# Performance work log

Hardware: AMD Instinct MI355X
Metric: run time of the kernel (lower is better)

Reference implementation:

```python
import jax, jax.numpy as jnp
import numpy as np

NUM_HEADS = 8


def setup_inputs() -> dict:
    key = jax.random.key(0)
    ks = jax.random.split(key, 5)
    b, c, h, w = 8, 256, 32, 32
    x = jax.random.normal(ks[0], (b, c, h, w), dtype=jnp.float32)
    w_qkv = jax.random.normal(ks[1], (3 * c, c), dtype=jnp.float32) * (c ** -0.5)
    b_qkv = jax.random.normal(ks[2], (3 * c,), dtype=jnp.float32) * 0.02
    w_proj = jax.random.normal(ks[3], (c, c), dtype=jnp.float32) * (c ** -0.5)
    b_proj = jax.random.normal(ks[4], (c,), dtype=jnp.float32) * 0.02
    return {"x": x, "w_qkv": w_qkv, "b_qkv": b_qkv, "w_proj": w_proj, "b_proj": b_proj}


def reference(x, w_qkv, b_qkv, w_proj, b_proj):
    b, c, h, w = x.shape
    nh = NUM_HEADS
    dh = c // nh
    L = h * w
    scale = dh ** -0.5
    # 1x1 conv == per-pixel GEMM
    qkv = jnp.einsum('bchw,oc->bohw', x, w_qkv) + b_qkv[None, :, None, None]
    qkv = qkv.reshape(b, 3, nh, dh, L)
    q, k, v = qkv[:, 0], qkv[:, 1], qkv[:, 2]  # each (b, nh, dh, L)
    attn = jnp.einsum('bhdi,bhdj->bhij', q, k) * scale  # (b, nh, L, L)
    attn = jax.nn.softmax(attn, axis=-1)
    out = jnp.einsum('bhdj,bhij->bhdi', v, attn)  # (b, nh, dh, L)
    out = out.reshape(b, c, h, w)
    proj = jnp.einsum('bchw,oc->bohw', out, w_proj) + b_proj[None, :, None, None]
    return x + proj
```

## Files before the change

kernel.cpp:

```cpp
#include <hip/hip_runtime.h>
#include <math.h>

#define B_   8
#define CIN  256
#define L_   1024
#define NH_  8
#define DH_  32

typedef __attribute__((ext_vector_type(8))) short short8;
typedef __attribute__((ext_vector_type(4))) short short4v;
typedef __attribute__((ext_vector_type(4))) float f32x4;
typedef __attribute__((ext_vector_type(4))) unsigned int uint4v;
typedef __attribute__((ext_vector_type(2))) unsigned int uint2v;

__device__ inline short f2bf_hu(float f) {
    union { float f; unsigned u; } v; v.f = f;
    return (short)((v.u + 0x8000u) >> 16);
}
__device__ inline float bf2f(short s) {
    union { unsigned u; float f; } v; v.u = ((unsigned)(unsigned short)s) << 16;
    return v.f;
}
__device__ inline unsigned pkbf2(float a, float b) {
    union { float f; unsigned u; } x, y; x.f = a; y.f = b;
    return __builtin_amdgcn_perm(y.u + 0x8000u, x.u + 0x8000u, 0x07060302u);
}
__device__ inline void glds16(const void* g, void* l) {
    __builtin_amdgcn_global_load_lds(
        (const __attribute__((address_space(1))) void*)g,
        (__attribute__((address_space(3))) void*)l, 16, 0, 0);
}

__global__ __launch_bounds__(256) void wconv(
    const float* __restrict__ wq, const float* __restrict__ wp,
    short* __restrict__ w2)
{
    const size_t e = ((size_t)blockIdx.x * 256 + threadIdx.x) * 8;
    const float* src = (e < (size_t)768 * 256) ? wq + e : wp + (e - (size_t)768 * 256);
    const float4 a = *(const float4*)src;
    const float4 c = *(const float4*)(src + 4);
    uint4v pk = { pkbf2(a.x, a.y), pkbf2(a.z, a.w),
                  pkbf2(c.x, c.y), pkbf2(c.z, c.w) };
    *(uint4v*)(w2 + e) = pk;
}

__global__ __launch_bounds__(256) void qkv_gemm(
    const float* __restrict__ x, const short* __restrict__ w2,
    const float* __restrict__ bias, short* __restrict__ qkvT)
{
    __shared__ __align__(16) short Xs[2][64][40];
    __shared__ __align__(16) short Wt[2][128][32];
    const int t = threadIdx.x, lane = t & 63, wv = t >> 6;
    const int n = lane & 15, quad = lane >> 4;
    const int b = blockIdx.z, o0 = blockIdx.y * 128, l0 = blockIdx.x * 64;

    float bias_r[8];
    #pragma unroll
    for (int nf = 0; nf < 8; nf++) bias_r[nf] = bias[o0 + nf * 16 + n];

    f32x4 acc[8];
    #pragma unroll
    for (int nf = 0; nf < 8; nf++) acc[nf] = (f32x4){0.f, 0.f, 0.f, 0.f};

    const int cS = t >> 3, lsS = (t & 7) * 8;

    const int oA = wv * 32 + (lane >> 2);
    const int cc = (lane & 3) ^ ((oA >> 1) & 3);
    const short* wpA = w2 + (size_t)(o0 + oA) * 256 + cc * 8;
    const short* wpB = wpA + 16 * 256;
    short* const ldsW0 = &Wt[0][0][0] + wv * 1024;
    short* const ldsW1 = &Wt[1][0][0] + wv * 1024;

    auto xwrite = [&](int buf, const float4& a, const float4& c) {
        const float vals[8] = {a.x, a.y, a.z, a.w, c.x, c.y, c.z, c.w};
        #pragma unroll
        for (int k = 0; k < 8; k++) {
            const int ll = lsS + k;
            const int col = (((cS >> 3) ^ (ll & 3)) << 3) | (cS & 7);
            Xs[buf][ll][col] = f2bf_hu(vals[k]);
        }
    };

    const float* xp = &x[(((size_t)b * CIN + cS) << 10) + l0 + lsS];
    float4 xa = *(const float4*)xp, xb = *(const float4*)(xp + 4);
    glds16(wpA, ldsW0);
    glds16(wpB, ldsW0 + 512);
    xwrite(0, xa, xb);
    xp += (size_t)32 << 10;
    xa = *(const float4*)xp; xb = *(const float4*)(xp + 4);

    const int wsw = (quad ^ ((n >> 1) & 3)) * 8;
    const int arow = wv * 16 + n;
    const int xsw = (quad ^ (arow & 3)) * 8;

    #pragma unroll
    for (int it = 0; it < 8; it++) {
        const int cur = it & 1;
        __syncthreads();
        if (it < 7) {
            short* ldsn = (cur ? ldsW0 : ldsW1);
            glds16(wpA + (it + 1) * 32, ldsn);
            glds16(wpB + (it + 1) * 32, ldsn + 512);
        }
        const short8 af = *(const short8*)&Xs[cur][arow][xsw];
        #pragma unroll
        for (int nf = 0; nf < 8; nf++) {
            const short8 bf = *(const short8*)&Wt[cur][nf * 16 + n][wsw];
            acc[nf] = __builtin_amdgcn_mfma_f32_16x16x32_bf16(af, bf, acc[nf], 0, 0, 0);
        }
        if (it < 7) {
            xwrite(cur ^ 1, xa, xb);
            if (it < 6) {
                xp += (size_t)32 << 10;
                xa = *(const float4*)xp; xb = *(const float4*)(xp + 4);
            }
        }
    }

    #pragma unroll
    for (int reg = 0; reg < 4; reg++) {
        const size_t l = l0 + wv * 16 + quad * 4 + reg;
        short* row = qkvT + (((size_t)b << 10) + l) * 768 + o0 + n;
        #pragma unroll
        for (int nf = 0; nf < 8; nf++)
            row[nf * 16] = f2bf_hu(acc[nf][reg] + bias_r[nf]);
    }
}

__global__ __launch_bounds__(256) void proj_gemm(
    const short* __restrict__ partO, const float* __restrict__ partD,
    const short* __restrict__ w2, const float* __restrict__ bias,
    const float* __restrict__ resid, float* __restrict__ out)
{
    __shared__ __align__(16) short Xs[2][64][40];
    __shared__ __align__(16) short Wt[2][64][32];
    const int t = threadIdx.x, lane = t & 63, wv = t >> 6;
    const int n = lane & 15, quad = lane >> 4;
    const int b = blockIdx.z, o0 = blockIdx.y * 64, l0 = blockIdx.x * 64;

    float bias_r[4];
    #pragma unroll
    for (int reg = 0; reg < 4; reg++) bias_r[reg] = bias[o0 + wv * 16 + quad * 4 + reg];

    f32x4 acc[4];
    #pragma unroll
    for (int nf = 0; nf < 4; nf++) acc[nf] = (f32x4){0.f, 0.f, 0.f, 0.f};

    const int l = t >> 2, cs = (t & 3) * 8;
    const size_t li = ((size_t)b << 10) + l0 + l;
    const short* p0 = &partO[(0 * (size_t)B_ * L_ + li) * CIN + cs];
    const short* p1 = &partO[(1 * (size_t)B_ * L_ + li) * CIN + cs];
    const float* pd0 = &partD[(0 * (size_t)B_ * L_ + li) * NH_];
    const float* pd1 = &partD[(1 * (size_t)B_ * L_ + li) * NH_];

    const int og = wv * 16 + (lane >> 2);
    const int ccg = (lane & 3) ^ ((og >> 1) & 3);
    const short* wp = w2 + (size_t)(o0 + og) * 256 + ccg * 8;
    short* const ldsW0 = &Wt[0][0][0] + wv * 512;
    short* const ldsW1 = &Wt[1][0][0] + wv * 512;

    short8 s0, s1;
    float d0, d1;
    auto combine_write = [&](int buf) {
        const float inv = 1.f / (d0 + d1);
        float v[8];
        #pragma unroll
        for (int e = 0; e < 8; e++) v[e] = (bf2f(s0[e]) + bf2f(s1[e])) * inv;
        uint4v pw = { pkbf2(v[0], v[1]), pkbf2(v[2], v[3]),
                      pkbf2(v[4], v[5]), pkbf2(v[6], v[7]) };
        *(uint4v*)&Xs[buf][l][cs] = pw;
    };

    s0 = *(const short8*)p0; s1 = *(const short8*)p1;
    d0 = pd0[0]; d1 = pd1[0];
    glds16(wp, ldsW0);
    combine_write(0);
    p0 += 32; p1 += 32;
    s0 = *(const short8*)p0; s1 = *(const short8*)p1;
    d0 = pd0[1]; d1 = pd1[1];

    const int wsw = (quad ^ ((n >> 1) & 3)) * 8;
    #pragma unroll
    for (int it = 0; it < 8; it++) {
        const int cur = it & 1;
        __syncthreads();
        if (it < 7) glds16(wp + (it + 1) * 32, cur ? ldsW0 : ldsW1);
        const short8 af = *(const short8*)&Wt[cur][wv * 16 + n][wsw];
        #pragma unroll
        for (int nf = 0; nf < 4; nf++) {
            const short8 bf = *(const short8*)&Xs[cur][nf * 16 + n][quad * 8];
            acc[nf] = __builtin_amdgcn_mfma_f32_16x16x32_bf16(af, bf, acc[nf], 0, 0, 0);
        }
        if (it < 7) {
            combine_write(cur ^ 1);
            if (it < 6) {
                p0 += 32; p1 += 32;
                s0 = *(const short8*)p0; s1 = *(const short8*)p1;
                d0 = pd0[it + 2]; d1 = pd1[it + 2];
            }
        }
    }

    #pragma unroll
    for (int reg = 0; reg < 4; reg++) {
        const int o = o0 + wv * 16 + quad * 4 + reg;
        #pragma unroll
        for (int nf = 0; nf < 4; nf++) {
            const size_t off = (((size_t)b * CIN + o) << 10) + l0 + nf * 16 + n;
            out[off] = acc[nf][reg] + bias_r[reg] + resid[off];
        }
    }
}

__global__ __launch_bounds__(256) void attn_mfma(
    const short* __restrict__ qkvT, short* __restrict__ partO,
    float* __restrict__ partD)
{
    __shared__ short Vt[2][32][80];
    __shared__ __align__(16) short Ss[128][88];

    const int t = threadIdx.x, lane = t & 63, wv = t >> 6;
    const int n = lane & 15, quad = lane >> 4;
    const int id = blockIdx.x;
    const int bh = id & 63;
    const int b = bh >> 3, h = bh & 7;
    const int i0 = ((id >> 6) & 7) * 128;
    const int s  = id >> 9;

    const short* base = qkvT + ((size_t)b << 10) * 768;

    short8 qa[2];
    #pragma unroll
    for (int a = 0; a < 2; a++)
        qa[a] = *(const short8*)&base[(size_t)(i0 + wv * 32 + a * 16 + n) * 768
                                      + h * DH_ + quad * 8];

    short8 vf2;
    {
        const short one = (n == 0) ? (short)0x3F80 : (short)0;
        #pragma unroll
        for (int u = 0; u < 8; u++) vf2[u] = one;
    }

    f32x4 o_acc[2][3];
    #pragma unroll
    for (int a = 0; a < 2; a++)
        #pragma unroll
        for (int nf = 0; nf < 3; nf++) o_acc[a][nf] = (f32x4){0.f, 0.f, 0.f, 0.f};

    const float K1 = 0.25503510f;
    const float K2 = 11.54156036f;
    const int TSTRIDE = 64 * 768;

    const size_t soff = (size_t)s * 8 * TSTRIDE;
    const short* kp0 = base + 256 + h * DH_ + (size_t)n * 768 + quad * 8 + soff;
    const short* kp1 = kp0 + 16 * 768;
    const short* kp2 = kp0 + 32 * 768;
    const short* kp3 = kp0 + 48 * 768;
    const int jS = t >> 3, dsS = (t & 7) * 4;
    const short* vp0 = base + 512 + h * DH_ + (size_t)jS * 768 + dsS + soff;
    const short* vp1 = vp0 + 32 * 768;

    const int vmsk = ((dsS >> 2) & 7) << 3;
    const int vwo0 = dsS * 80 + (jS ^ vmsk);
    const int vwo1 = dsS * 80 + ((jS + 32) ^ vmsk);
    short* const vtb0 = &Vt[0][0][0];
    short* const vtb1 = &Vt[1][0][0];
    short* const ssw  = &Ss[wv * 32 + n][quad * 4];
    const short* const ssr = &Ss[wv * 32 + n][quad * 8];
    int vro[2][2];
    #pragma unroll
    for (int nf = 0; nf < 2; nf++) {
        const int dv = nf * 16 + n;
        const int msk = ((dv >> 2) & 7) << 3;
        #pragma unroll
        for (int kk = 0; kk < 2; kk++)
            vro[kk][nf] = dv * 80 + ((kk * 32 + quad * 8) ^ msk);
    }

    short8 kfA[4], kfB[4];

    auto stageV = [&](short* vtb) {
        const short4v a = *(const short4v*)vp0; vp0 += TSTRIDE;
        const short4v c = *(const short4v*)vp1; vp1 += TSTRIDE;
        #pragma unroll
        for (int u = 0; u < 4; u++) {
            vtb[vwo0 + u * 80] = a[u];
            vtb[vwo1 + u * 80] = c[u];
        }
    };
    auto loadK = [&](short8* kf) {
        kf[0] = *(const short8*)kp0; kp0 += TSTRIDE;
        kf[1] = *(const short8*)kp1; kp1 += TSTRIDE;
        kf[2] = *(const short8*)kp2; kp2 += TSTRIDE;
        kf[3] = *(const short8*)kp3; kp3 += TSTRIDE;
    };
    auto tile = [&](const short8* kf, const short* vtb) {
        #pragma unroll
        for (int f = 0; f < 4; f++) {
            #pragma unroll
            for (int a = 0; a < 2; a++) {
                f32x4 z = {0.f, 0.f, 0.f, 0.f};
                const f32x4 sv = __builtin_amdgcn_mfma_f32_16x16x32_bf16(kf[f], qa[a], z, 0, 0, 0);
                const float p0 = __builtin_amdgcn_exp2f(fmaf(sv[0], K1, -K2));
                const float p1 = __builtin_amdgcn_exp2f(fmaf(sv[1], K1, -K2));
                const float p2 = __builtin_amdgcn_exp2f(fmaf(sv[2], K1, -K2));
                const float p3 = __builtin_amdgcn_exp2f(fmaf(sv[3], K1, -K2));
                uint2v pk = { pkbf2(p0, p1), pkbf2(p2, p3) };
                *(uint2v*)(ssw + a * 16 * 88 + f * 16) = pk;
            }
        }
        #pragma unroll
        for (int kk = 0; kk < 2; kk++) {
            short8 pf[2];
            #pragma unroll
            for (int a = 0; a < 2; a++)
                pf[a] = *(const short8*)(ssr + a * 16 * 88 + kk * 32);
            #pragma unroll
            for (int nf = 0; nf < 2; nf++) {
                const short8 vf = *(const short8*)(vtb + vro[kk][nf]);
                #pragma unroll
                for (int a = 0; a < 2; a++)
                    o_acc[a][nf] = __builtin_amdgcn_mfma_f32_16x16x32_bf16(pf[a], vf, o_acc[a][nf], 0, 0, 0);
            }
            #pragma unroll
            for (int a = 0; a < 2; a++)
                o_acc[a][2] = __builtin_amdgcn_mfma_f32_16x16x32_bf16(pf[a], vf2, o_acc[a][2], 0, 0, 0);
        }
    };

    stageV(vtb0);
    loadK(kfA);

    for (int itp = 0; itp < 4; itp++) {
        __syncthreads();
        stageV(vtb1);
        loadK(kfB);
        tile(kfA, vtb0);
        __syncthreads();
        if (itp < 3) { stageV(vtb0); loadK(kfA); }
        tile(kfB, vtb1);
    }

    #pragma unroll
    for (int a = 0; a < 2; a++) {
        #pragma unroll
        for (int r = 0; r < 4; r++) {
            const int il = i0 + wv * 32 + a * 16 + quad * 4 + r;
            short* po = partO + (((size_t)s * B_ + b) * L_ + il) * CIN + h * DH_;
            po[n]      = f2bf_hu(o_acc[a][0][r]);
            po[16 + n] = f2bf_hu(o_acc[a][1][r]);
        }
    }
    if (n == 0) {
        #pragma unroll
        for (int a = 0; a < 2; a++)
            #pragma unroll
            for (int r = 0; r < 4; r++) {
                const int il = i0 + wv * 32 + a * 16 + quad * 4 + r;
                partD[(((size_t)s * B_ + b) * L_ + il) * NH_ + h] = o_acc[a][2][r];
            }
    }
}

extern "C" void kernel_launch(void* const* d_in, const int* in_sizes, int n_in,
                              void* d_out, int out_size, void* d_ws, size_t ws_size,
                              hipStream_t stream) {
    const float* x      = (const float*)d_in[0];
    const float* w_qkv  = (const float*)d_in[1];
    const float* b_qkv  = (const float*)d_in[2];
    const float* w_proj = (const float*)d_in[3];
    const float* b_proj = (const float*)d_in[4];
    float* out = (float*)d_out;

    short* qkvT  = (short*)d_ws;
    short* partO = qkvT + (size_t)B_ * L_ * 768;
    float* partD = (float*)(partO + (size_t)2 * B_ * L_ * CIN);
    short* w2    = (short*)(partD + (size_t)2 * B_ * L_ * NH_);

    wconv<<<dim3(128), 256, 0, stream>>>(w_qkv, w_proj, w2);
    qkv_gemm<<<dim3(16, 6, B_), 256, 0, stream>>>(x, w2, b_qkv, qkvT);
    attn_mfma<<<dim3(1024), 256, 0, stream>>>(qkvT, partO, partD);
    proj_gemm<<<dim3(16, 4, B_), 256, 0, stream>>>(partO, partD, w2 + (size_t)768 * 256,
                                                   b_proj, x, out);
}
```

Measured before the change: 111.9 us.

## Drop split-K attention partials; use 64-query tiles over full key range

The attention kernel previously split the key dimension into two halves and had each block handle 128 queries, writing bf16 partial outputs and fp32 denominators that the projection GEMM then combined. Now each block handles 64 queries (16 per wave) over all 1024 keys, normalizes in-register and writes a single bf16 O buffer, so proj_gemm just loads it directly. This removes the partial-output traffic and the combine arithmetic but halves K/V reuse per block and doubles the serial loop length per block.

```diff
diff --git a/kernel.cpp b/kernel.cpp
--- a/kernel.cpp
+++ b/kernel.cpp
@@ -127,138 +127,42 @@
     }
 }
 
-__global__ __launch_bounds__(256) void proj_gemm(
-    const short* __restrict__ partO, const float* __restrict__ partD,
-    const short* __restrict__ w2, const float* __restrict__ bias,
-    const float* __restrict__ resid, float* __restrict__ out)
-{
-    __shared__ __align__(16) short Xs[2][64][40];
-    __shared__ __align__(16) short Wt[2][64][32];
-    const int t = threadIdx.x, lane = t & 63, wv = t >> 6;
-    const int n = lane & 15, quad = lane >> 4;
-    const int b = blockIdx.z, o0 = blockIdx.y * 64, l0 = blockIdx.x * 64;
-
-    float bias_r[4];
-    #pragma unroll
-    for (int reg = 0; reg < 4; reg++) bias_r[reg] = bias[o0 + wv * 16 + quad * 4 + reg];
-
-    f32x4 acc[4];
-    #pragma unroll
-    for (int nf = 0; nf < 4; nf++) acc[nf] = (f32x4){0.f, 0.f, 0.f, 0.f};
-
-    const int l = t >> 2, cs = (t & 3) * 8;
-    const size_t li = ((size_t)b << 10) + l0 + l;
-    const short* p0 = &partO[(0 * (size_t)B_ * L_ + li) * CIN + cs];
-    const short* p1 = &partO[(1 * (size_t)B_ * L_ + li) * CIN + cs];
-    const float* pd0 = &partD[(0 * (size_t)B_ * L_ + li) * NH_];
-    const float* pd1 = &partD[(1 * (size_t)B_ * L_ + li) * NH_];
-
-    const int og = wv * 16 + (lane >> 2);
-    const int ccg = (lane & 3) ^ ((og >> 1) & 3);
-    const short* wp = w2 + (size_t)(o0 + og) * 256 + ccg * 8;
-    short* const ldsW0 = &Wt[0][0][0] + wv * 512;
-    short* const ldsW1 = &Wt[1][0][0] + wv * 512;
-
-    short8 s0, s1;
-    float d0, d1;
-    auto combine_write = [&](int buf) {
-        const float inv = 1.f / (d0 + d1);
-        float v[8];
-        #pragma unroll
-        for (int e = 0; e < 8; e++) v[e] = (bf2f(s0[e]) + bf2f(s1[e])) * inv;
-        uint4v pw = { pkbf2(v[0], v[1]), pkbf2(v[2], v[3]),
-                      pkbf2(v[4], v[5]), pkbf2(v[6], v[7]) };
-        *(uint4v*)&Xs[buf][l][cs] = pw;
-    };
-
-    s0 = *(const short8*)p0; s1 = *(const short8*)p1;
-    d0 = pd0[0]; d1 = pd1[0];
-    glds16(wp, ldsW0);
-    combine_write(0);
-    p0 += 32; p1 += 32;
-    s0 = *(const short8*)p0; s1 = *(const short8*)p1;
-    d0 = pd0[1]; d1 = pd1[1];
-
-    const int wsw = (quad ^ ((n >> 1) & 3)) * 8;
-    #pragma unroll
-    for (int it = 0; it < 8; it++) {
-        const int cur = it & 1;
-        __syncthreads();
-        if (it < 7) glds16(wp + (it + 1) * 32, cur ? ldsW0 : ldsW1);
-        const short8 af = *(const short8*)&Wt[cur][wv * 16 + n][wsw];
-        #pragma unroll
-        for (int nf = 0; nf < 4; nf++) {
-            const short8 bf = *(const short8*)&Xs[cur][nf * 16 + n][quad * 8];
-            acc[nf] = __builtin_amdgcn_mfma_f32_16x16x32_bf16(af, bf, acc[nf], 0, 0, 0);
-        }
-        if (it < 7) {
-            combine_write(cur ^ 1);
-            if (it < 6) {
-                p0 += 32; p1 += 32;
-                s0 = *(const short8*)p0; s1 = *(const short8*)p1;
-                d0 = pd0[it + 2]; d1 = pd1[it + 2];
-            }
-        }
-    }
-
-    #pragma unroll
-    for (int reg = 0; reg < 4; reg++) {
-        const int o = o0 + wv * 16 + quad * 4 + reg;
-        #pragma unroll
-        for (int nf = 0; nf < 4; nf++) {
-            const size_t off = (((size_t)b * CIN + o) << 10) + l0 + nf * 16 + n;
-            out[off] = acc[nf][reg] + bias_r[reg] + resid[off];
-        }
-    }
-}
-
 __global__ __launch_bounds__(256) void attn_mfma(
-    const short* __restrict__ qkvT, short* __restrict__ partO,
-    float* __restrict__ partD)
+    const short* __restrict__ qkvT, short* __restrict__ O)
 {
     __shared__ short Vt[2][32][80];
-    __shared__ __align__(16) short Ss[128][88];
+    __shared__ __align__(16) short Ss[64][88];
 
     const int t = threadIdx.x, lane = t & 63, wv = t >> 6;
     const int n = lane & 15, quad = lane >> 4;
     const int id = blockIdx.x;
     const int bh = id & 63;
     const int b = bh >> 3, h = bh & 7;
-    const int i0 = ((id >> 6) & 7) * 128;
-    const int s  = id >> 9;
+    const int i0 = (id >> 6) * 64;
 
     const short* base = qkvT + ((size_t)b << 10) * 768;
 
-    short8 qa[2];
-    #pragma unroll
-    for (int a = 0; a < 2; a++)
-        qa[a] = *(const short8*)&base[(size_t)(i0 + wv * 32 + a * 16 + n) * 768
-                                      + h * DH_ + quad * 8];
+    const short8 qa = *(const short8*)&base[(size_t)(i0 + wv * 16 + n) * 768
+                                            + h * DH_ + quad * 8];
 
     short8 vf2;
-    {
-        const short one = (n == 0) ? (short)0x3F80 : (short)0;
-        #pragma unroll
-        for (int u = 0; u < 8; u++) vf2[u] = one;
-    }
-
-    f32x4 o_acc[2][3];
-    #pragma unroll
-    for (int a = 0; a < 2; a++)
-        #pragma unroll
-        for (int nf = 0; nf < 3; nf++) o_acc[a][nf] = (f32x4){0.f, 0.f, 0.f, 0.f};
+    #pragma unroll
+    for (int u = 0; u < 8; u++) vf2[u] = (short)0x3F80;
+
+    f32x4 o_acc[3];
+    #pragma unroll
+    for (int nf = 0; nf < 3; nf++) o_acc[nf] = (f32x4){0.f, 0.f, 0.f, 0.f};
 
     const float K1 = 0.25503510f;
     const float K2 = 11.54156036f;
     const int TSTRIDE = 64 * 768;
 
-    const size_t soff = (size_t)s * 8 * TSTRIDE;
-    const short* kp0 = base + 256 + h * DH_ + (size_t)n * 768 + quad * 8 + soff;
+    const short* kp0 = base + 256 + h * DH_ + (size_t)n * 768 + quad * 8;
     const short* kp1 = kp0 + 16 * 768;
     const short* kp2 = kp0 + 32 * 768;
     const short* kp3 = kp0 + 48 * 768;
     const int jS = t >> 3, dsS = (t & 7) * 4;
-    const short* vp0 = base + 512 + h * DH_ + (size_t)jS * 768 + dsS + soff;
+    const short* vp0 = base + 512 + h * DH_ + (size_t)jS * 768 + dsS;
     const short* vp1 = vp0 + 32 * 768;
 
     const int vmsk = ((dsS >> 2) & 7) << 3;
@@ -266,8 +170,8 @@
     const int vwo1 = dsS * 80 + ((jS + 32) ^ vmsk);
     short* const vtb0 = &Vt[0][0][0];
     short* const vtb1 = &Vt[1][0][0];
-    short* const ssw  = &Ss[wv * 32 + n][quad * 4];
-    const short* const ssr = &Ss[wv * 32 + n][quad * 8];
+    short* const ssw  = &Ss[wv * 16 + n][quad * 4];
+    const short* const ssr = &Ss[wv * 16 + n][quad * 8];
     int vro[2][2];
     #pragma unroll
     for (int nf = 0; nf < 2; nf++) {
@@ -298,68 +202,116 @@
     auto tile = [&](const short8* kf, const short* vtb) {
         #pragma unroll
         for (int f = 0; f < 4; f++) {
-            #pragma unroll
-            for (int a = 0; a < 2; a++) {
-                f32x4 z = {0.f, 0.f, 0.f, 0.f};
-                const f32x4 sv = __builtin_amdgcn_mfma_f32_16x16x32_bf16(kf[f], qa[a], z, 0, 0, 0);
-                const float p0 = __builtin_amdgcn_exp2f(fmaf(sv[0], K1, -K2));
-                const float p1 = __builtin_amdgcn_exp2f(fmaf(sv[1], K1, -K2));
-                const float p2 = __builtin_amdgcn_exp2f(fmaf(sv[2], K1, -K2));
-                const float p3 = __builtin_amdgcn_exp2f(fmaf(sv[3], K1, -K2));
-                uint2v pk = { pkbf2(p0, p1), pkbf2(p2, p3) };
-                *(uint2v*)(ssw + a * 16 * 88 + f * 16) = pk;
-            }
+            f32x4 z = {0.f, 0.f, 0.f, 0.f};
+            const f32x4 sv = __builtin_amdgcn_mfma_f32_16x16x32_bf16(kf[f], qa, z, 0, 0, 0);
+            const float p0 = __builtin_amdgcn_exp2f(fmaf(sv[0], K1, -K2));
+            const float p1 = __builtin_amdgcn_exp2f(fmaf(sv[1], K1, -K2));
+            const float p2 = __builtin_amdgcn_exp2f(fmaf(sv[2], K1, -K2));
+            const float p3 = __builtin_amdgcn_exp2f(fmaf(sv[3], K1, -K2));
+            uint2v pk = { pkbf2(p0, p1), pkbf2(p2, p3) };
+            *(uint2v*)(ssw + f * 16) = pk;
         }
         #pragma unroll
         for (int kk = 0; kk < 2; kk++) {
-            short8 pf[2];
-            #pragma unroll
-            for (int a = 0; a < 2; a++)
-                pf[a] = *(const short8*)(ssr + a * 16 * 88 + kk * 32);
+            const short8 pf = *(const short8*)(ssr + kk * 32);
             #pragma unroll
             for (int nf = 0; nf < 2; nf++) {
                 const short8 vf = *(const short8*)(vtb + vro[kk][nf]);
-                #pragma unroll
-                for (int a = 0; a < 2; a++)
-                    o_acc[a][nf] = __builtin_amdgcn_mfma_f32_16x16x32_bf16(pf[a], vf, o_acc[a][nf], 0, 0, 0);
+                o_acc[nf] = __builtin_amdgcn_mfma_f32_16x16x32_bf16(pf, vf, o_acc[nf], 0, 0, 0);
             }
-            #pragma unroll
-            for (int a = 0; a < 2; a++)
-                o_acc[a][2] = __builtin_amdgcn_mfma_f32_16x16x32_bf16(pf[a], vf2, o_acc[a][2], 0, 0, 0);
+            o_acc[2] = __builtin_amdgcn_mfma_f32_16x16x32_bf16(pf, vf2, o_acc[2], 0, 0, 0);
         }
     };
 
     stageV(vtb0);
     loadK(kfA);
 
-    for (int itp = 0; itp < 4; itp++) {
+    for (int itp = 0; itp < 8; itp++) {
         __syncthreads();
         stageV(vtb1);
         loadK(kfB);
         tile(kfA, vtb0);
         __syncthreads();
-        if (itp < 3) { stageV(vtb0); loadK(kfA); }
+        if (itp < 7) { stageV(vtb0); loadK(kfA); }
         tile(kfB, vtb1);
     }
 
     #pragma unroll
-    for (int a = 0; a < 2; a++) {
-        #pragma unroll
-        for (int r = 0; r < 4; r++) {
-            const int il = i0 + wv * 32 + a * 16 + quad * 4 + r;
-            short* po = partO + (((size_t)s * B_ + b) * L_ + il) * CIN + h * DH_;
-            po[n]      = f2bf_hu(o_acc[a][0][r]);
-            po[16 + n] = f2bf_hu(o_acc[a][1][r]);
-        }
-    }
-    if (n == 0) {
-        #pragma unroll
-        for (int a = 0; a < 2; a++)
-            #pragma unroll
-            for (int r = 0; r < 4; r++) {
-                const int il = i0 + wv * 32 + a * 16 + quad * 4 + r;
-                partD[(((size_t)s * B_ + b) * L_ + il) * NH_ + h] = o_acc[a][2][r];
+    for (int r = 0; r < 4; r++) {
+        const float inv = 1.f / o_acc[2][r];
+        const int il = i0 + wv * 16 + quad * 4 + r;
+        short* po = O + (((size_t)b << 10) + il) * CIN + h * DH_;
+        po[n]      = f2bf_hu(o_acc[0][r] * inv);
+        po[16 + n] = f2bf_hu(o_acc[1][r] * inv);
+    }
+}
+
+__global__ __launch_bounds__(256) void proj_gemm(
+    const short* __restrict__ O, const short* __restrict__ w2,
+    const float* __restrict__ bias, const float* __restrict__ resid,
+    float* __restrict__ out)
+{
+    __shared__ __align__(16) short Xs[2][64][40];
+    __shared__ __align__(16) short Wt[2][64][32];
+    const int t = threadIdx.x, lane = t & 63, wv = t >> 6;
+    const int n = lane & 15, quad = lane >> 4;
+    const int b = blockIdx.z, o0 = blockIdx.y * 64, l0 = blockIdx.x * 64;
+
+    float bias_r[4];
+    #pragma unroll
+    for (int reg = 0; reg < 4; reg++) bias_r[reg] = bias[o0 + wv * 16 + quad * 4 + reg];
+
+    f32x4 acc[4];
+    #pragma unroll
+    for (int nf = 0; nf < 4; nf++) acc[nf] = (f32x4){0.f, 0.f, 0.f, 0.f};
+
+    const int l = t >> 2, cs = (t & 3) * 8;
+    const short* p0 = &O[(((size_t)b << 10) + l0 + l) * CIN + cs];
+
+    const int og = wv * 16 + (lane >> 2);
+    const int ccg = (lane & 3) ^ ((og >> 1) & 3);
+    const short* wp = w2 + (size_t)(o0 + og) * 256 + ccg * 8;
+    short* const ldsW0 = &Wt[0][0][0] + wv * 512;
+    short* const ldsW1 = &Wt[1][0][0] + wv * 512;
+
+    short8 s0;
+    auto xwrite = [&](int buf) { *(short8*)&Xs[buf][l][cs] = s0; };
+
+    s0 = *(const short8*)p0;
+    glds16(wp, ldsW0);
+    xwrite(0);
+    p0 += 32;
+    s0 = *(const short8*)p0;
+
+    const int wsw = (quad ^ ((n >> 1) & 3)) * 8;
+    #pragma unroll
+    for (int it = 0; it < 8; it++) {
+        const int cur = it & 1;
+        __syncthreads();
+        if (it < 7) glds16(wp + (it + 1) * 32, cur ? ldsW0 : ldsW1);
+        const short8 af = *(const short8*)&Wt[cur][wv * 16 + n][wsw];
+        #pragma unroll
+        for (int nf = 0; nf < 4; nf++) {
+            const short8 bf = *(const short8*)&Xs[cur][nf * 16 + n][quad * 8];
+            acc[nf] = __builtin_amdgcn_mfma_f32_16x16x32_bf16(af, bf, acc[nf], 0, 0, 0);
+        }
+        if (it < 7) {
+            xwrite(cur ^ 1);
+            if (it < 6) {
+                p0 += 32;
+                s0 = *(const short8*)p0;
             }
+        }
+    }
+
+    #pragma unroll
+    for (int reg = 0; reg < 4; reg++) {
+        const int o = o0 + wv * 16 + quad * 4 + reg;
+        #pragma unroll
+        for (int nf = 0; nf < 4; nf++) {
+            const size_t off = (((size_t)b * CIN + o) << 10) + l0 + nf * 16 + n;
+            out[off] = acc[nf][reg] + bias_r[reg] + resid[off];
+        }
     }
 }
 
@@ -373,14 +325,13 @@
     const float* b_proj = (const float*)d_in[4];
     float* out = (float*)d_out;
 
-    short* qkvT  = (short*)d_ws;
-    short* partO = qkvT + (size_t)B_ * L_ * 768;
-    float* partD = (float*)(partO + (size_t)2 * B_ * L_ * CIN);
-    short* w2    = (short*)(partD + (size_t)2 * B_ * L_ * NH_);
+    short* qkvT = (short*)d_ws;
+    short* Obuf = qkvT + (size_t)B_ * L_ * 768;
+    short* w2   = Obuf + (size_t)B_ * L_ * CIN;
 
     wconv<<<dim3(128), 256, 0, stream>>>(w_qkv, w_proj, w2);
     qkv_gemm<<<dim3(16, 6, B_), 256, 0, stream>>>(x, w2, b_qkv, qkvT);
-    attn_mfma<<<dim3(1024), 256, 0, stream>>>(qkvT, partO, partD);
-    proj_gemm<<<dim3(16, 4, B_), 256, 0, stream>>>(partO, partD, w2 + (size_t)768 * 256,
+    attn_mfma<<<dim3(1024), 256, 0, stream>>>(qkvT, Obuf);
+    proj_gemm<<<dim3(16, 4, B_), 256, 0, stream>>>(Obuf, w2 + (size_t)768 * 256,
                                                    b_proj, x, out);
 }
```

Result: slower. 124.5 us (+11.2%).
